# Kernel tuning notes

Measured on AMD Instinct MI355X. Metric: run time of the kernel, lower is better.

The kernel has to match this reference:

```python
import jax, jax.numpy as jnp
import numpy as np


def _rope(x):
    # x: [..., T, hs]
    T, hs = x.shape[-2], x.shape[-1]
    pos = jnp.arange(T, dtype=x.dtype)[:, None]                      # [T,1]
    theta = 1.0 / (10000.0 ** (jnp.arange(0, hs, 2, dtype=x.dtype) / hs))  # [hs/2]
    ang = pos * theta                                                # [T, hs/2]
    cos, sin = jnp.cos(ang), jnp.sin(ang)
    x1, x2 = x[..., 0::2], x[..., 1::2]
    out = jnp.stack([x1 * cos - x2 * sin, x1 * sin + x2 * cos], axis=-1)
    return out.reshape(x.shape)


def _layernorm(x, w, b, eps=1e-5):
    mu = jnp.mean(x, axis=-1, keepdims=True)
    var = jnp.mean(jnp.square(x - mu), axis=-1, keepdims=True)
    return (x - mu) * jax.lax.rsqrt(var + eps) * w + b


def setup_inputs() -> dict:
    key = jax.random.key(0)
    ks = jax.random.split(key, 8)
    B, T, D, H, HS = 8, 1024, 1024, 16, 64
    s = lambda fan: 1.0 / np.sqrt(fan)
    return {
        'x': jax.random.normal(ks[0], (B, T, D), jnp.float32),
        'wq': jax.random.normal(ks[1], (H, D, HS), jnp.float32) * s(D),
        'wk': jax.random.normal(ks[2], (H, D, HS), jnp.float32) * s(D),
        'wv': jax.random.normal(ks[3], (H, D, HS), jnp.float32) * s(D),
        'w_proj': jax.random.normal(ks[4], (D, D), jnp.float32) * s(D),
        'b_proj': jnp.zeros((D,), jnp.float32),
        'ln1_w': jnp.ones((D,), jnp.float32),
        'ln1_b': jnp.zeros((D,), jnp.float32),
        'ln2_w': jnp.ones((D,), jnp.float32),
        'ln2_b': jnp.zeros((D,), jnp.float32),
        'w1': jax.random.normal(ks[5], (D, 4 * D), jnp.float32) * s(D),
        'b1': jnp.zeros((4 * D,), jnp.float32),
        'w2': jax.random.normal(ks[6], (4 * D, D), jnp.float32) * s(4 * D),
        'b2': jnp.zeros((D,), jnp.float32),
    }


def reference(x, wq, wk, wv, w_proj, b_proj, ln1_w, ln1_b, ln2_w, ln2_b, w1, b1, w2, b2):
    B, T, D = x.shape
    H, _, HS = wq.shape
    # --- attention sub-block (pre-LN, causal, RoPE on q/k) ---
    xn = _layernorm(x, ln1_w, ln1_b)
    q = jnp.einsum('btd,hdk->bhtk', xn, wq)   # [B,H,T,HS]
    k = jnp.einsum('btd,hdk->bhtk', xn, wk)
    v = jnp.einsum('btd,hdk->bhtk', xn, wv)
    q = _rope(q)
    k = _rope(k)
    scores = jnp.einsum('bhqk,bhsk->bhqs', q, k) * (HS ** -0.5)  # [B,H,T,T]
    causal = jnp.tril(jnp.ones((T, T), bool))
    scores = jnp.where(causal, scores, -jnp.inf)
    attn = jax.nn.softmax(scores, axis=-1)
    o = jnp.einsum('bhqs,bhsk->bhqk', attn, v)                   # [B,H,T,HS]
    o = jnp.transpose(o, (0, 2, 1, 3)).reshape(B, T, H * HS)     # concat heads
    x = x + o @ w_proj + b_proj                                  # dropout is identity in eval
    # --- FFN sub-block ---
    xn2 = _layernorm(x, ln2_w, ln2_b)
    h = jax.nn.relu(xn2 @ w1 + b1)
    x = x + h @ w2 + b2
    return x
```

## Files before the change

### kernel.cpp

```cpp
#include <hip/hip_runtime.h>
#include <hip/hip_bf16.h>
#include <math.h>

#define DEV static __device__ __forceinline__

typedef __attribute__((ext_vector_type(8))) __bf16 bf16x8;
typedef __attribute__((ext_vector_type(4))) float f32x4;
typedef __attribute__((ext_vector_type(8))) unsigned short ushort8;
typedef __attribute__((ext_vector_type(4))) unsigned short ushort4v;

#define Bb 8
#define Tt 1024
#define Dd 1024
#define Hh 16
#define HS 64
#define BT 8192
#define DFF 4096
#define QS 8388608ull

DEV unsigned short f2bf(float f) {
  union { float f; unsigned int u; } v; v.f = f;
  unsigned int r = v.u + 0x7fffu + ((v.u >> 16) & 1u);
  return (unsigned short)(r >> 16);
}
DEV float bf2f(unsigned short h) {
  union { unsigned int u; float f; } v; v.u = ((unsigned int)h) << 16;
  return v.f;
}

DEV void gload_lds16(const void* g, void* l) {
  __builtin_amdgcn_global_load_lds(
      (const __attribute__((address_space(1))) void*)g,
      (__attribute__((address_space(3))) void*)l, 16, 0, 0);
}

__global__ void rope_tab_k(float2* __restrict__ tab) {
  int idx = blockIdx.x * 256 + threadIdx.x;
  int t = idx >> 5, i = idx & 31;
  float theta = exp2f(-(float)i * (13.287712379549449f / 32.f));
  float sn, cs;
  sincosf((float)t * theta, &sn, &cs);
  tab[idx] = make_float2(cs, sn);
}

__global__ __launch_bounds__(256) void pack_qkv_t(const float* __restrict__ wq,
                                                  const float* __restrict__ wk,
                                                  const float* __restrict__ wv,
                                                  unsigned short* __restrict__ dst) {
  __shared__ float tile[32][33];
  int z = blockIdx.z, which = z >> 4, hh = z & 15;
  const float* src = which == 0 ? wq : (which == 1 ? wk : wv);
  int d0 = blockIdx.y * 32, hs0 = blockIdx.x * 32;
  int c = threadIdx.x & 31, r8 = threadIdx.x >> 5;
  #pragma unroll
  for (int r = 0; r < 4; ++r) {
    int d = d0 + r8 + r * 8;
    tile[r8 + r * 8][c] = src[((size_t)hh * Dd + d) * HS + hs0 + c];
  }
  __syncthreads();
  #pragma unroll
  for (int r = 0; r < 4; ++r) {
    int hs = hs0 + r8 + r * 8;
    dst[((size_t)which * 1024 + hh * 64 + hs) * Dd + d0 + c] = f2bf(tile[c][r8 + r * 8]);
  }
}

__global__ __launch_bounds__(256) void pack_t_tiled(const float* __restrict__ src,
                                                    unsigned short* __restrict__ dst,
                                                    int N, int K) {
  __shared__ float tile[32][33];
  int n0 = blockIdx.x * 32, k0 = blockIdx.y * 32;
  int c = threadIdx.x & 31, r8 = threadIdx.x >> 5;
  #pragma unroll
  for (int r = 0; r < 4; ++r)
    tile[r8 + r * 8][c] = src[(size_t)(k0 + r8 + r * 8) * N + n0 + c];
  __syncthreads();
  #pragma unroll
  for (int r = 0; r < 4; ++r)
    dst[(size_t)(n0 + r8 + r * 8) * K + k0 + c] = f2bf(tile[c][r8 + r * 8]);
}

__global__ __launch_bounds__(256) void ln_k(const float* __restrict__ in,
                                            const float* __restrict__ w,
                                            const float* __restrict__ b,
                                            unsigned short* __restrict__ out) {
  __shared__ float sbuf[8];
  int row = blockIdx.x, t = threadIdx.x;
  const float4 v = ((const float4*)(in + (size_t)row * Dd))[t];
  float s = v.x + v.y + v.z + v.w;
  float q = v.x * v.x + v.y * v.y + v.z * v.z + v.w * v.w;
  #pragma unroll
  for (int o = 32; o > 0; o >>= 1) { s += __shfl_down(s, o); q += __shfl_down(q, o); }
  if ((t & 63) == 0) { sbuf[t >> 6] = s; sbuf[4 + (t >> 6)] = q; }
  __syncthreads();
  s = (sbuf[0] + sbuf[1]) + (sbuf[2] + sbuf[3]);
  q = (sbuf[4] + sbuf[5]) + (sbuf[6] + sbuf[7]);
  float mu = s * (1.f / Dd);
  float var = q * (1.f / Dd) - mu * mu;
  float inv = rsqrtf(var + 1e-5f);
  const float4 wv = ((const float4*)w)[t];
  const float4 bv = ((const float4*)b)[t];
  ushort4v r;
  r[0] = f2bf((v.x - mu) * inv * wv.x + bv.x);
  r[1] = f2bf((v.y - mu) * inv * wv.y + bv.y);
  r[2] = f2bf((v.z - mu) * inv * wv.z + bv.z);
  r[3] = f2bf((v.w - mu) * inv * wv.w + bv.w);
  *(ushort4v*)&out[(size_t)row * Dd + t * 4] = r;
}

__global__ __launch_bounds__(256) void ln_bf_k(const unsigned short* __restrict__ in,
                                               const float* __restrict__ w,
                                               const float* __restrict__ b,
                                               unsigned short* __restrict__ out) {
  __shared__ float sbuf[8];
  int row = blockIdx.x, t = threadIdx.x;
  ushort4v hv = *(const ushort4v*)&in[(size_t)row * Dd + t * 4];
  float e0 = bf2f(hv[0]), e1 = bf2f(hv[1]), e2 = bf2f(hv[2]), e3 = bf2f(hv[3]);
  float s = e0 + e1 + e2 + e3;
  float q = e0 * e0 + e1 * e1 + e2 * e2 + e3 * e3;
  #pragma unroll
  for (int o = 32; o > 0; o >>= 1) { s += __shfl_down(s, o); q += __shfl_down(q, o); }
  if ((t & 63) == 0) { sbuf[t >> 6] = s; sbuf[4 + (t >> 6)] = q; }
  __syncthreads();
  s = (sbuf[0] + sbuf[1]) + (sbuf[2] + sbuf[3]);
  q = (sbuf[4] + sbuf[5]) + (sbuf[6] + sbuf[7]);
  float mu = s * (1.f / Dd);
  float var = q * (1.f / Dd) - mu * mu;
  float inv = rsqrtf(var + 1e-5f);
  const float4 wv = ((const float4*)w)[t];
  const float4 bv = ((const float4*)b)[t];
  ushort4v r;
  r[0] = f2bf((e0 - mu) * inv * wv.x + bv.x);
  r[1] = f2bf((e1 - mu) * inv * wv.y + bv.y);
  r[2] = f2bf((e2 - mu) * inv * wv.z + bv.z);
  r[3] = f2bf((e3 - mu) * inv * wv.w + bv.w);
  *(ushort4v*)&out[(size_t)row * Dd + t * 4] = r;
}

template <int MODE>
__global__ __launch_bounds__(256) void gemm_bk64(
    const unsigned short* __restrict__ A, const unsigned short* __restrict__ Bt,
    int M, int N, int K,
    const float* __restrict__ bias, const float* __restrict__ resid,
    const unsigned short* __restrict__ residb,
    float* __restrict__ outf, unsigned short* __restrict__ outb) {
  __shared__ __align__(16) unsigned short As[2][128 * 64];
  __shared__ __align__(16) unsigned short Bs[2][128 * 64];
  const int tid = threadIdx.x;
  const int lane = tid & 63, wave = tid >> 6;
  const int l15 = lane & 15, lg = lane >> 4;
  const int wm = wave >> 1, wn = wave & 1;
  const int sw = l15 & 7;

  int orig = blockIdx.y * gridDim.x + blockIdx.x;
  int xcd = orig & 7, c = orig >> 3;
  int w = c & 63, g = c >> 6;
  int bx = g * 8 + (w & 7);
  int by = xcd * 8 + (w >> 3);
  const int brow = by * 128, bcol = bx * 128;

  const unsigned short* Ag = A + (size_t)brow * K;
  const unsigned short* Bg = Bt + (size_t)bcol * K;
  const int NT = K >> 6;

  int stg_off[4];
  #pragma unroll
  for (int j = 0; j < 4; ++j) {
    int idx = j * 256 + tid;
    int r = idx >> 3, slot = idx & 7;
    stg_off[j] = r * K + ((slot ^ (r & 7)) * 8);
  }
  int aoff[4][2], boff[4][2];
  #pragma unroll
  for (int mi = 0; mi < 4; ++mi)
    #pragma unroll
    for (int kk = 0; kk < 2; ++kk) {
      aoff[mi][kk] = (((wm * 64 + mi * 16 + l15) * 64) + (((kk * 4 + lg) ^ sw) * 8)) * 2;
      boff[mi][kk] = (((wn * 64 + mi * 16 + l15) * 64) + (((kk * 4 + lg) ^ sw) * 8)) * 2;
    }

#define STAGE_T(k0_, buf_)                                                        \
  do {                                                                            \
    _Pragma("unroll")                                                             \
    for (int j = 0; j < 4; ++j) {                                                 \
      gload_lds16(Ag + stg_off[j] + (k0_), &As[buf_][(size_t)(j * 256 + tid) * 8]); \
      gload_lds16(Bg + stg_off[j] + (k0_), &Bs[buf_][(size_t)(j * 256 + tid) * 8]); \
    }                                                                             \
  } while (0)

  STAGE_T(0, 0);
  asm volatile("s_waitcnt vmcnt(0)" ::: "memory");
  __builtin_amdgcn_s_barrier();

  f32x4 acc[4][4] = {};

  for (int t = 0; t < NT; ++t) {
    const char* Abuf = (const char*)As[t & 1];
    const char* Bbuf = (const char*)Bs[t & 1];
    if (t + 1 < NT) STAGE_T((t + 1) * 64, (t + 1) & 1);
    bf16x8 af[4][2], bf[4][2];
    #pragma unroll
    for (int mi = 0; mi < 4; ++mi)
      #pragma unroll
      for (int kk = 0; kk < 2; ++kk) {
        af[mi][kk] = *(const bf16x8*)(Abuf + aoff[mi][kk]);
        bf[mi][kk] = *(const bf16x8*)(Bbuf + boff[mi][kk]);
      }
    __builtin_amdgcn_s_setprio(1);
    #pragma unroll
    for (int kk = 0; kk < 2; ++kk)
      #pragma unroll
      for (int mi = 0; mi < 4; ++mi)
        #pragma unroll
        for (int ni = 0; ni < 4; ++ni)
          acc[mi][ni] = __builtin_amdgcn_mfma_f32_16x16x32_bf16(af[mi][kk], bf[ni][kk], acc[mi][ni], 0, 0, 0);
    __builtin_amdgcn_s_setprio(0);
    if (t + 1 < NT) asm volatile("s_waitcnt vmcnt(0)" ::: "memory");
    __builtin_amdgcn_s_barrier();
  }
#undef STAGE_T

  #pragma unroll
  for (int m = 0; m < 4; ++m) {
    #pragma unroll
    for (int n = 0; n < 4; ++n) {
      int row0 = brow + wm * 64 + m * 16 + lg * 4;
      int col = bcol + wn * 64 + n * 16 + l15;
      if constexpr (MODE == 0) {
        int b = row0 >> 10, t0 = row0 & 1023;
        int which = col >> 10, rem = col & 1023, hh = rem >> 6, hs = rem & 63;
        if (which == 2) {
          uint2 pk;
          pk.x = (unsigned int)f2bf(acc[m][n][0]) | ((unsigned int)f2bf(acc[m][n][1]) << 16);
          pk.y = (unsigned int)f2bf(acc[m][n][2]) | ((unsigned int)f2bf(acc[m][n][3]) << 16);
          *(uint2*)&outb[2 * QS + ((size_t)(b * Hh + hh) * HS + hs) * Tt + t0] = pk;
        } else {
          const float2* tab = (const float2*)bias;
          float qs = (which == 0) ? 0.18033688f : 1.0f;
          float sgn = ((hs & 1) == 0) ? -1.0f : 1.0f;
          #pragma unroll
          for (int r = 0; r < 4; ++r) {
            float own = acc[m][n][r];
            float partner = __shfl_xor(own, 1);
            float2 cssn = tab[(size_t)(t0 + r) * 32 + (hs >> 1)];
            float val = (cssn.x * own + sgn * cssn.y * partner) * qs;
            outb[(size_t)which * QS + ((size_t)((b * Hh + hh) * Tt + t0 + r)) * HS + hs] =
                f2bf(val);
          }
        }
      } else if constexpr (MODE == 1) {
        #pragma unroll
        for (int r = 0; r < 4; ++r)
          outf[(size_t)(row0 + r) * N + col] =
              bf2f(residb[(size_t)(row0 + r) * N + col]) + acc[m][n][r] + bias[col];
      } else if constexpr (MODE == 2) {
        #pragma unroll
        for (int r = 0; r < 4; ++r) {
          float z = acc[m][n][r] + bias[col];
          outb[(size_t)(row0 + r) * N + col] = f2bf(z > 0.f ? z : 0.f);
        }
      } else {
        #pragma unroll
        for (int r = 0; r < 4; ++r)
          outb[(size_t)(row0 + r) * N + col] =
              f2bf(resid[(size_t)(row0 + r) * N + col] + acc[m][n][r] + bias[col]);
      }
    }
  }
}

__global__ __launch_bounds__(256) void attn_k(const unsigned short* __restrict__ qkv,
                                              unsigned short* __restrict__ O) {
  __shared__ __align__(16) unsigned short K_lds[2][64 * 64];
  __shared__ __align__(16) unsigned short Vt_lds[2][64 * 64];
  __shared__ __align__(16) unsigned short P_lds[4][32 * 64];
  const int tid = threadIdx.x;
  const int wave = tid >> 6, lane = tid & 63;
  const int l15 = lane & 15, lg = lane >> 4;
  const int sw = l15 & 7;
  const int bh = blockIdx.x;
  const int q0 = (7 - (int)blockIdx.y) * 128;
  const int qw0 = q0 + wave * 32;

  bf16x8 qf[2][2];
  {
    const unsigned short* Qg = qkv + ((size_t)bh * Tt + qw0 + l15) * HS;
    #pragma unroll
    for (int qi = 0; qi < 2; ++qi)
      #pragma unroll
      for (int dg = 0; dg < 2; ++dg)
        qf[qi][dg] = *(const bf16x8*)&Qg[(size_t)qi * 16 * HS + dg * 32 + lg * 8];
  }
  f32x4 oacc[2][4] = {};
  float m_r[2] = {-1e30f, -1e30f};
  float l_r[2] = {0.f, 0.f};

  const unsigned short* Kg = qkv + QS + (size_t)bh * Tt * HS;
  const unsigned short* Vg = qkv + 2 * QS + (size_t)bh * HS * Tt;

  const int srow = lane >> 3;
  const int scol = ((lane & 7) ^ (srow & 7)) * 8;
  const int i0 = wave * 2, i1 = wave * 2 + 1;

#define STAGE_KV(s0_, buf_)                                                        \
  do {                                                                             \
    gload_lds16(Kg + (size_t)((s0_) + i0 * 8 + srow) * HS + scol,                  \
                (char*)&K_lds[buf_][0] + i0 * 1024);                               \
    gload_lds16(Kg + (size_t)((s0_) + i1 * 8 + srow) * HS + scol,                  \
                (char*)&K_lds[buf_][0] + i1 * 1024);                               \
    gload_lds16(Vg + (size_t)(i0 * 8 + srow) * Tt + (s0_) + scol,                  \
                (char*)&Vt_lds[buf_][0] + i0 * 1024);                              \
    gload_lds16(Vg + (size_t)(i1 * 8 + srow) * Tt + (s0_) + scol,                  \
                (char*)&Vt_lds[buf_][0] + i1 * 1024);                              \
  } while (0)

  const int nsteps = (q0 + 128) >> 6;
  STAGE_KV(0, 0);

  for (int t = 0; t < nsteps; ++t) {
    const int s0 = t << 6;
    if (t + 1 < nsteps) {
      STAGE_KV(s0 + 64, (t + 1) & 1);
      asm volatile("s_waitcnt vmcnt(4)" ::: "memory");
    } else {
      asm volatile("s_waitcnt vmcnt(0)" ::: "memory");
    }
    __builtin_amdgcn_s_barrier();

    const unsigned short* Kb = K_lds[t & 1];
    const unsigned short* Vb = Vt_lds[t & 1];

    if (s0 <= qw0 + 31) {
      f32x4 st[4][2];
      #pragma unroll
      for (int si = 0; si < 4; ++si) {
        bf16x8 kf0 = *(const bf16x8*)&Kb[(size_t)(si * 16 + l15) * 64 + ((lg ^ sw) * 8)];
        bf16x8 kf1 = *(const bf16x8*)&Kb[(size_t)(si * 16 + l15) * 64 + (((4 + lg) ^ sw) * 8)];
        #pragma unroll
        for (int qi = 0; qi < 2; ++qi) {
          f32x4 a = {};
          a = __builtin_amdgcn_mfma_f32_16x16x32_bf16(kf0, qf[qi][0], a, 0, 0, 0);
          a = __builtin_amdgcn_mfma_f32_16x16x32_bf16(kf1, qf[qi][1], a, 0, 0, 0);
          st[si][qi] = a;
        }
      }
      if (s0 + 63 > qw0) {
        #pragma unroll
        for (int si = 0; si < 4; ++si)
          #pragma unroll
          for (int qi = 0; qi < 2; ++qi) {
            int base = (s0 + si * 16 + lg * 4) - (qw0 + qi * 16 + l15);
            #pragma unroll
            for (int r = 0; r < 4; ++r)
              if (base + r > 0) st[si][qi][r] = -1e30f;
          }
      }
      #pragma unroll
      for (int qi = 0; qi < 2; ++qi) {
        float ms[4];
        #pragma unroll
        for (int si = 0; si < 4; ++si)
          ms[si] = fmaxf(fmaxf(st[si][qi][0], st[si][qi][1]),
                         fmaxf(st[si][qi][2], st[si][qi][3]));
        float pm = fmaxf(fmaxf(ms[0], ms[1]), fmaxf(ms[2], ms[3]));
        pm = fmaxf(pm, __shfl_xor(pm, 16));
        pm = fmaxf(pm, __shfl_xor(pm, 32));
        if (__any(pm - m_r[qi] > 8.f)) {
          float mn = fmaxf(m_r[qi], pm);
          float corr = __builtin_amdgcn_exp2f(m_r[qi] - mn);
          m_r[qi] = mn;
          l_r[qi] *= corr;
          #pragma unroll
          for (int r = 0; r < 4; ++r) {
            float c = __shfl(corr, (lane & 48) + lg * 4 + r);
            #pragma unroll
            for (int dj = 0; dj < 4; ++dj) oacc[qi][dj][r] *= c;
          }
        }
        float rs = 0.f;
        #pragma unroll
        for (int si = 0; si < 4; ++si) {
          #pragma unroll
          for (int r = 0; r < 4; ++r) {
            float p = __builtin_amdgcn_exp2f(st[si][qi][r] - m_r[qi]);
            st[si][qi][r] = p;
            rs += p;
          }
        }
        rs += __shfl_xor(rs, 16);
        rs += __shfl_xor(rs, 32);
        l_r[qi] += rs;
        #pragma unroll
        for (int si = 0; si < 4; ++si) {
          uint2 pk;
          asm("v_cvt_pk_bf16_f32 %0, %1, %2"
              : "=v"(pk.x) : "v"(st[si][qi][0]), "v"(st[si][qi][1]));
          asm("v_cvt_pk_bf16_f32 %0, %1, %2"
              : "=v"(pk.y) : "v"(st[si][qi][2]), "v"(st[si][qi][3]));
          int slot = si * 2 + (lg >> 1);
          *(uint2*)&P_lds[wave][(size_t)(qi * 16 + l15) * 64 + ((slot ^ sw) * 8) + (lg & 1) * 4] = pk;
        }
      }
      bf16x8 pf[2][2];
      #pragma unroll
      for (int qi = 0; qi < 2; ++qi)
        #pragma unroll
        for (int sg = 0; sg < 2; ++sg)
          pf[qi][sg] = *(const bf16x8*)&P_lds[wave][(size_t)(qi * 16 + l15) * 64 + (((sg * 4 + lg) ^ sw) * 8)];
      #pragma unroll
      for (int dj = 0; dj < 4; ++dj) {
        bf16x8 vf0 = *(const bf16x8*)&Vb[(size_t)(dj * 16 + l15) * 64 + ((lg ^ sw) * 8)];
        bf16x8 vf1 = *(const bf16x8*)&Vb[(size_t)(dj * 16 + l15) * 64 + (((4 + lg) ^ sw) * 8)];
        #pragma unroll
        for (int qi = 0; qi < 2; ++qi) {
          oacc[qi][dj] = __builtin_amdgcn_mfma_f32_16x16x32_bf16(pf[qi][0], vf0, oacc[qi][dj], 0, 0, 0);
          oacc[qi][dj] = __builtin_amdgcn_mfma_f32_16x16x32_bf16(pf[qi][1], vf1, oacc[qi][dj], 0, 0, 0);
        }
      }
    }
    __builtin_amdgcn_s_barrier();
  }
#undef STAGE_KV

  int b = bh >> 4, hh = bh & 15;
  #pragma unroll
  for (int qi = 0; qi < 2; ++qi) {
    float linv = 1.f / l_r[qi];
    #pragma unroll
    for (int r = 0; r < 4; ++r) {
      float li = __shfl(linv, (lane & 48) + lg * 4 + r);
      int qg = qw0 + qi * 16 + lg * 4 + r;
      unsigned short* Og = O + ((size_t)(b * Tt + qg)) * Dd + hh * HS;
      #pragma unroll
      for (int dj = 0; dj < 4; ++dj)
        Og[dj * 16 + l15] = f2bf(oacc[qi][dj][r] * li);
    }
  }
}

extern "C" void kernel_launch(void* const* d_in, const int* in_sizes, int n_in,
                              void* d_out, int out_size, void* d_ws, size_t ws_size,
                              hipStream_t stream) {
  const float* x      = (const float*)d_in[0];
  const float* wq     = (const float*)d_in[1];
  const float* wk     = (const float*)d_in[2];
  const float* wv     = (const float*)d_in[3];
  const float* w_proj = (const float*)d_in[4];
  const float* b_proj = (const float*)d_in[5];
  const float* ln1_w  = (const float*)d_in[6];
  const float* ln1_b  = (const float*)d_in[7];
  const float* ln2_w  = (const float*)d_in[8];
  const float* ln2_b  = (const float*)d_in[9];
  const float* w1     = (const float*)d_in[10];
  const float* b1     = (const float*)d_in[11];
  const float* w2     = (const float*)d_in[12];
  const float* b2     = (const float*)d_in[13];
  float* out = (float*)d_out;

  char* ws = (char*)d_ws;
  unsigned short* Wt_qkv  = (unsigned short*)(ws + 0);
  unsigned short* Wt_proj = (unsigned short*)(ws + 6291456);
  unsigned short* Wt_1    = (unsigned short*)(ws + 8388608);
  unsigned short* Wt_2    = (unsigned short*)(ws + 16777216);
  unsigned short* x1b     = (unsigned short*)(ws + 25165824);
  unsigned short* xn      = (unsigned short*)(ws + 58720256);
  unsigned short* qkv     = (unsigned short*)(ws + 75497472);
  unsigned short* O       = (unsigned short*)(ws + 125829120);
  unsigned short* xn2     = O;
  unsigned short* hbuf    = (unsigned short*)(ws + 58720256);
  float*          rtab    = (float*)(ws + 141557760);

  rope_tab_k<<<128, 256, 0, stream>>>((float2*)rtab);
  pack_qkv_t<<<dim3(2, 32, 48), 256, 0, stream>>>(wq, wk, wv, Wt_qkv);
  pack_t_tiled<<<dim3(32, 32), 256, 0, stream>>>(w_proj, Wt_proj, 1024, 1024);
  pack_t_tiled<<<dim3(128, 32), 256, 0, stream>>>(w1, Wt_1, 4096, 1024);
  pack_t_tiled<<<dim3(32, 128), 256, 0, stream>>>(w2, Wt_2, 1024, 4096);

  ln_k<<<BT, 256, 0, stream>>>(x, ln1_w, ln1_b, xn);

  gemm_bk64<0><<<dim3(24, 64), 256, 0, stream>>>(xn, Wt_qkv, BT, 3072, 1024,
                                                 rtab, nullptr, nullptr, nullptr, qkv);

  attn_k<<<dim3(128, 8), 256, 0, stream>>>(qkv, O);

  gemm_bk64<3><<<dim3(8, 64), 256, 0, stream>>>(O, Wt_proj, BT, 1024, 1024,
                                                b_proj, x, nullptr, nullptr, x1b);
  ln_bf_k<<<BT, 256, 0, stream>>>(x1b, ln2_w, ln2_b, xn2);

  gemm_bk64<2><<<dim3(32, 64), 256, 0, stream>>>(xn2, Wt_1, BT, 4096, 1024,
                                                 b1, nullptr, nullptr, nullptr, hbuf);
  gemm_bk64<1><<<dim3(8, 64), 256, 0, stream>>>(hbuf, Wt_2, BT, 1024, 4096,
                                                b2, nullptr, x1b, out, nullptr);
}
```

Baseline: 333.4 us.

## Retile GEMMs to 128x256 tiles with BK=32 and 8 waves per block

The GEMM kernel moves from 256-thread blocks on 128x128 tiles with K-step 64 to 512-thread blocks on 128x256 tiles with K-step 32. A new paired-row swizzled LDS layout keeps 16-byte loads conflict-free at the narrower K width. The XCD-aware block remap is reworked to suit the new grid shapes. The wider N tile cuts A-operand global traffic and raises the block's arithmetic intensity, but the smaller K-step doubles the number of barriers per unit of work, and launch bounds of 512 threads with 4 blocks limit registers.

```diff
diff --git a/kernel.cpp b/kernel.cpp
--- a/kernel.cpp
+++ b/kernel.cpp
@@ -137,55 +137,60 @@
   *(ushort4v*)&out[(size_t)row * Dd + t * 4] = r;
 }
 
+DEV int pr_stage_off(int idx, int ldK) {
+  int R = idx >> 3, s = idx & 7;
+  int L = s ^ (R & 7);
+  int mrow = 2 * R + (L >> 2);
+  int kg = L & 3;
+  return mrow * ldK + kg * 8;
+}
+DEV int pr_frag_off(int r, int lgi) {
+  int R = r >> 1;
+  int s = ((r & 1) * 4 + lgi) ^ (R & 7);
+  return (R * 64 + s * 8) * 2;
+}
+
 template <int MODE>
-__global__ __launch_bounds__(256) void gemm_bk64(
+__global__ __launch_bounds__(512, 4) void gemm_bk32(
     const unsigned short* __restrict__ A, const unsigned short* __restrict__ Bt,
     int M, int N, int K,
     const float* __restrict__ bias, const float* __restrict__ resid,
     const unsigned short* __restrict__ residb,
     float* __restrict__ outf, unsigned short* __restrict__ outb) {
-  __shared__ __align__(16) unsigned short As[2][128 * 64];
-  __shared__ __align__(16) unsigned short Bs[2][128 * 64];
+  __shared__ __align__(16) unsigned short As[2][4096];
+  __shared__ __align__(16) unsigned short Bs[2][8192];
   const int tid = threadIdx.x;
   const int lane = tid & 63, wave = tid >> 6;
   const int l15 = lane & 15, lg = lane >> 4;
-  const int wm = wave >> 1, wn = wave & 1;
-  const int sw = l15 & 7;
-
-  int orig = blockIdx.y * gridDim.x + blockIdx.x;
+  const int wm = wave >> 2, wn = wave & 3;
+
+  int gx = gridDim.x;
+  int orig = blockIdx.y * gx + blockIdx.x;
   int xcd = orig & 7, c = orig >> 3;
-  int w = c & 63, g = c >> 6;
-  int bx = g * 8 + (w & 7);
-  int by = xcd * 8 + (w >> 3);
-  const int brow = by * 128, bcol = bx * 128;
+  int bx = c % gx;
+  int by = xcd * 8 + (c / gx);
+  const int brow = by * 128, bcol = bx * 256;
 
   const unsigned short* Ag = A + (size_t)brow * K;
   const unsigned short* Bg = Bt + (size_t)bcol * K;
-  const int NT = K >> 6;
-
-  int stg_off[4];
-  #pragma unroll
-  for (int j = 0; j < 4; ++j) {
-    int idx = j * 256 + tid;
-    int r = idx >> 3, slot = idx & 7;
-    stg_off[j] = r * K + ((slot ^ (r & 7)) * 8);
-  }
-  int aoff[4][2], boff[4][2];
-  #pragma unroll
-  for (int mi = 0; mi < 4; ++mi)
-    #pragma unroll
-    for (int kk = 0; kk < 2; ++kk) {
-      aoff[mi][kk] = (((wm * 64 + mi * 16 + l15) * 64) + (((kk * 4 + lg) ^ sw) * 8)) * 2;
-      boff[mi][kk] = (((wn * 64 + mi * 16 + l15) * 64) + (((kk * 4 + lg) ^ sw) * 8)) * 2;
-    }
-
-#define STAGE_T(k0_, buf_)                                                        \
-  do {                                                                            \
-    _Pragma("unroll")                                                             \
-    for (int j = 0; j < 4; ++j) {                                                 \
-      gload_lds16(Ag + stg_off[j] + (k0_), &As[buf_][(size_t)(j * 256 + tid) * 8]); \
-      gload_lds16(Bg + stg_off[j] + (k0_), &Bs[buf_][(size_t)(j * 256 + tid) * 8]); \
-    }                                                                             \
+  const int NT = K >> 5;
+
+  const int stgA  = pr_stage_off(tid, K);
+  const int stgB0 = pr_stage_off(tid, K);
+  const int stgB1 = pr_stage_off(512 + tid, K);
+
+  int aoff[4], boff[4];
+  #pragma unroll
+  for (int i = 0; i < 4; ++i) {
+    aoff[i] = pr_frag_off(wm * 64 + i * 16 + l15, lg);
+    boff[i] = pr_frag_off(wn * 64 + i * 16 + l15, lg);
+  }
+
+#define STAGE_T(k0_, buf_)                                                    \
+  do {                                                                        \
+    gload_lds16(Ag + stgA + (k0_), &As[buf_][(size_t)tid * 8]);               \
+    gload_lds16(Bg + stgB0 + (k0_), &Bs[buf_][(size_t)tid * 8]);              \
+    gload_lds16(Bg + stgB1 + (k0_), &Bs[buf_][(size_t)(512 + tid) * 8]);      \
   } while (0)
 
   STAGE_T(0, 0);
@@ -197,23 +202,19 @@
   for (int t = 0; t < NT; ++t) {
     const char* Abuf = (const char*)As[t & 1];
     const char* Bbuf = (const char*)Bs[t & 1];
-    if (t + 1 < NT) STAGE_T((t + 1) * 64, (t + 1) & 1);
-    bf16x8 af[4][2], bf[4][2];
+    if (t + 1 < NT) STAGE_T((t + 1) * 32, (t + 1) & 1);
+    bf16x8 af[4], bf[4];
+    #pragma unroll
+    for (int i = 0; i < 4; ++i) {
+      af[i] = *(const bf16x8*)(Abuf + aoff[i]);
+      bf[i] = *(const bf16x8*)(Bbuf + boff[i]);
+    }
+    __builtin_amdgcn_s_setprio(1);
     #pragma unroll
     for (int mi = 0; mi < 4; ++mi)
       #pragma unroll
-      for (int kk = 0; kk < 2; ++kk) {
-        af[mi][kk] = *(const bf16x8*)(Abuf + aoff[mi][kk]);
-        bf[mi][kk] = *(const bf16x8*)(Bbuf + boff[mi][kk]);
-      }
-    __builtin_amdgcn_s_setprio(1);
-    #pragma unroll
-    for (int kk = 0; kk < 2; ++kk)
-      #pragma unroll
-      for (int mi = 0; mi < 4; ++mi)
-        #pragma unroll
-        for (int ni = 0; ni < 4; ++ni)
-          acc[mi][ni] = __builtin_amdgcn_mfma_f32_16x16x32_bf16(af[mi][kk], bf[ni][kk], acc[mi][ni], 0, 0, 0);
+      for (int ni = 0; ni < 4; ++ni)
+        acc[mi][ni] = __builtin_amdgcn_mfma_f32_16x16x32_bf16(af[mi], bf[ni], acc[mi][ni], 0, 0, 0);
     __builtin_amdgcn_s_setprio(0);
     if (t + 1 < NT) asm volatile("s_waitcnt vmcnt(0)" ::: "memory");
     __builtin_amdgcn_s_barrier();
@@ -478,17 +479,17 @@
 
   ln_k<<<BT, 256, 0, stream>>>(x, ln1_w, ln1_b, xn);
 
-  gemm_bk64<0><<<dim3(24, 64), 256, 0, stream>>>(xn, Wt_qkv, BT, 3072, 1024,
+  gemm_bk32<0><<<dim3(12, 64), 512, 0, stream>>>(xn, Wt_qkv, BT, 3072, 1024,
                                                  rtab, nullptr, nullptr, nullptr, qkv);
 
   attn_k<<<dim3(128, 8), 256, 0, stream>>>(qkv, O);
 
-  gemm_bk64<3><<<dim3(8, 64), 256, 0, stream>>>(O, Wt_proj, BT, 1024, 1024,
+  gemm_bk32<3><<<dim3(4, 64), 512, 0, stream>>>(O, Wt_proj, BT, 1024, 1024,
                                                 b_proj, x, nullptr, nullptr, x1b);
   ln_bf_k<<<BT, 256, 0, stream>>>(x1b, ln2_w, ln2_b, xn2);
 
-  gemm_bk64<2><<<dim3(32, 64), 256, 0, stream>>>(xn2, Wt_1, BT, 4096, 1024,
+  gemm_bk32<2><<<dim3(16, 64), 512, 0, stream>>>(xn2, Wt_1, BT, 4096, 1024,
                                                  b1, nullptr, nullptr, nullptr, hbuf);
-  gemm_bk64<1><<<dim3(8, 64), 256, 0, stream>>>(hbuf, Wt_2, BT, 1024, 4096,
+  gemm_bk32<1><<<dim3(4, 64), 512, 0, stream>>>(hbuf, Wt_2, BT, 1024, 4096,
                                                 b2, nullptr, x1b, out, nullptr);
 }
```

After: 369.8 us. +10.9%, slower.
